# Optimization experiments

Hardware: AMD Instinct MI355X
Metric: run time of the kernel (lower is better)

Reference implementation:

```python
import jax, jax.numpy as jnp
import numpy as np

NC, NW, E, EW = 100000, 500, 600000, 25000
H, L, DFF, CF, WF = 128, 3, 512, 32, 16


def setup_inputs() -> dict:
    key = jax.random.key(0)
    ks = iter(jax.random.split(key, 48))
    def nrm(shape, s=0.05):
        return jax.random.normal(next(ks), shape, jnp.float32) * s
    inp = {}
    inp["cell_x"] = jax.random.normal(next(ks), (NC, CF), jnp.float32)
    inp["well_x"] = jax.random.normal(next(ks), (NW, WF), jnp.float32)
    inp["c2c_edge_index"] = jax.random.randint(next(ks), (2, E), 0, NC)
    inp["c2c_edge_attr"] = jax.random.normal(next(ks), (E, 1), jnp.float32)
    inp["c2w_src"] = jax.random.randint(next(ks), (EW,), 0, NC)
    inp["c2w_dst"] = jax.random.randint(next(ks), (EW,), 0, NW)
    inp["W_cell"] = nrm((CF, H)); inp["b_cell"] = jnp.zeros((H,), jnp.float32)
    inp["W_well"] = nrm((WF, H)); inp["b_well"] = jnp.zeros((H,), jnp.float32)
    inp["W_ee"] = nrm((1, H));   inp["b_ee"] = jnp.zeros((H,), jnp.float32)
    inp["gW"]  = nrm((L, H, H))
    inp["gas"] = nrm((L, H)); inp["gad"] = nrm((L, H)); inp["gae"] = nrm((L, H))
    inp["gWe"] = nrm((L, H, H)); inp["gb"] = jnp.zeros((L, H), jnp.float32)
    inp["n1g"] = jnp.ones((L, H), jnp.float32); inp["n1b"] = jnp.zeros((L, H), jnp.float32)
    inp["fW1"] = nrm((L, H, DFF)); inp["fb1"] = jnp.zeros((L, DFF), jnp.float32)
    inp["fW2"] = nrm((L, DFF, H)); inp["fb2"] = jnp.zeros((L, H), jnp.float32)
    inp["n2g"] = jnp.ones((L, H), jnp.float32); inp["n2b"] = jnp.zeros((L, H), jnp.float32)
    inp["wW"] = nrm((H, H)); inp["was"] = nrm((H,)); inp["wad"] = nrm((H,))
    inp["wb"] = jnp.zeros((H,), jnp.float32)
    inp["mW1"] = nrm((H, H)); inp["mb1"] = jnp.zeros((H,), jnp.float32)
    inp["mW2"] = nrm((H, 75)); inp["mb2"] = jnp.zeros((75,), jnp.float32)
    return inp


def _layer_norm(x, g, b):
    mu = x.mean(-1, keepdims=True)
    v = ((x - mu) ** 2).mean(-1, keepdims=True)
    return (x - mu) * jax.lax.rsqrt(v + 1e-5) * g + b


def _seg_softmax(a, seg, n):
    # numerically stable softmax over edges grouped by destination node
    m = jax.ops.segment_max(a, seg, num_segments=n)
    e = jnp.exp(a - m[seg])
    s = jax.ops.segment_sum(e, seg, num_segments=n)
    s = jnp.where(s == 0, 1.0, s)
    return e / s[seg]


def reference(cell_x, well_x, c2c_edge_index, c2c_edge_attr, c2w_src, c2w_dst,
              W_cell, b_cell, W_well, b_well, W_ee, b_ee,
              gW, gas, gad, gae, gWe, gb,
              n1g, n1b, fW1, fb1, fW2, fb2, n2g, n2b,
              wW, was, wad, wb, mW1, mb1, mW2, mb2):
    src, dst = c2c_edge_index[0], c2c_edge_index[1]
    h = cell_x @ W_cell + b_cell           # [NC, H]
    hw = well_x @ W_well + b_well          # [NW, H]
    ea = c2c_edge_attr @ W_ee + b_ee       # [E, H] embedded edge features
    for i in range(L):
        # GATConv with edge features (heads=1, concat=False, no self loops)
        xn = _layer_norm(h, n1g[i], n1b[i])
        hs = xn @ gW[i]                    # [NC, H]
        alpha = (hs @ gas[i])[src] + (hs @ gad[i])[dst] + (ea @ gWe[i]) @ gae[i]
        alpha = jax.nn.leaky_relu(alpha, 0.2)
        alpha = _seg_softmax(alpha, dst, NC)
        msg = jax.ops.segment_sum(hs[src] * alpha[:, None], dst, num_segments=NC) + gb[i]
        h = h + msg                        # residual (dropout = identity in eval)
        xn = _layer_norm(h, n2g[i], n2b[i])
        h = h + (jax.nn.relu(xn @ fW1[i] + fb1[i]) @ fW2[i] + fb2[i])
    # cell -> well bipartite GATConv (shared lin for src/dst, no edge feats)
    hc = h @ wW                            # [NC, H]
    hwp = hw @ wW                          # [NW, H]
    a = (hc @ was)[c2w_src] + (hwp @ wad)[c2w_dst]
    a = jax.nn.leaky_relu(a, 0.2)
    a = _seg_softmax(a, c2w_dst, NW)
    h_well = jax.ops.segment_sum(hc[c2w_src] * a[:, None], c2w_dst, num_segments=NW) + wb
    out = jax.nn.relu(h_well @ mW1 + mb1) @ mW2 + mb2
    return out.reshape(-1, 3, 25)
```

## Files before the change

### kernel.cpp

```cpp
#include <hip/hip_runtime.h>
#include <hip/hip_bf16.h>

#define NC 100000
#define NW 500
#define NE_CC 600000
#define NE_CW 25000
#define H 128
#define NL 3
#define DFF 512
#define DC 64

typedef __bf16 bf16x8 __attribute__((ext_vector_type(8)));
typedef float f32x4 __attribute__((ext_vector_type(4)));
#define MFMA16(a,b,c) __builtin_amdgcn_mfma_f32_16x16x32_bf16(a,b,c,0,0,0)

__device__ __forceinline__ float wsum(float v){
  #pragma unroll
  for (int o = 32; o; o >>= 1) v += __shfl_xor(v, o, 64);
  return v;
}
__device__ __forceinline__ float gsum16(float v){
  #pragma unroll
  for (int o = 1; o < 16; o <<= 1) v += __shfl_xor(v, o, 64);
  return v;
}
__device__ __forceinline__ float gmax16(float v){
  #pragma unroll
  for (int o = 1; o < 16; o <<= 1) v = fmaxf(v, __shfl_xor(v, o, 64));
  return v;
}

__device__ __forceinline__ void gload16(const void* g, void* l){
  __builtin_amdgcn_global_load_lds(
      (const __attribute__((address_space(1))) void*)g,
      (__attribute__((address_space(3))) void*)l, 16, 0, 0);
}


__global__ void prep_imgGW_k(const float* __restrict__ in, char* __restrict__ img, int nmat){
  int tot = nmat * 16384;
  for (int i = blockIdx.x * 256 + threadIdx.x; i < tot; i += gridDim.x * 256){
    int j = i & 7, lane = (i >> 3) & 63, f = (i >> 9) & 31, l = i >> 14;
    int lr = lane & 15, lk = lane >> 4;
    int ks = f >> 3, nt = f & 7;
    int k = ks * 32 + lk * 8 + j, n = nt * 16 + lr;
    float v = in[(size_t)l * 16384 + (size_t)k * 128 + n];
    *(__hip_bfloat16*)(img + (size_t)l * 32768 + f * 1024 + lane * 16 + j * 2) =
        __float2bfloat16(v);
  }
}
__global__ void prep_imgW1_k(const float* __restrict__ in, char* __restrict__ img){
  int tot = 3 * 65536;
  for (int i = blockIdx.x * 256 + threadIdx.x; i < tot; i += gridDim.x * 256){
    int j = i & 7, lane = (i >> 3) & 63, f = (i >> 9) & 15, ch = (i >> 13) & 7, l = i >> 16;
    int lr = lane & 15, lk = lane >> 4;
    int ks = f >> 2, nt = f & 3;
    int k = ks * 32 + lk * 8 + j, n = ch * 64 + nt * 16 + lr;
    float v = in[(size_t)l * 65536 + (size_t)k * 512 + n];
    *(__hip_bfloat16*)(img + (size_t)(l * 8 + ch) * 16384 + f * 1024 + lane * 16 + j * 2) =
        __float2bfloat16(v);
  }
}
__global__ void prep_imgW2_k(const float* __restrict__ in, char* __restrict__ img){
  int tot = 3 * 65536;
  for (int i = blockIdx.x * 256 + threadIdx.x; i < tot; i += gridDim.x * 256){
    int j = i & 7, lane = (i >> 3) & 63, f = (i >> 9) & 15, ch = (i >> 13) & 7, l = i >> 16;
    int lr = lane & 15, lk = lane >> 4;
    int ks = f >> 3, nt = f & 7;
    int k = ch * 64 + ks * 32 + lk * 8 + j, n = nt * 16 + lr;
    float v = in[(size_t)l * 65536 + (size_t)k * 128 + n];
    *(__hip_bfloat16*)(img + (size_t)(l * 8 + ch) * 16384 + f * 1024 + lane * 16 + j * 2) =
        __float2bfloat16(v);
  }
}

__global__ __launch_bounds__(256) void embed_ln_k(const float* __restrict__ x,
    const float* __restrict__ W, const float* __restrict__ b,
    const float* __restrict__ g, const float* __restrict__ lb,
    float* __restrict__ h, __hip_bfloat16* __restrict__ xn, int M)
{
  int lane = threadIdx.x & 63, wid = threadIdx.x >> 6;
  float w0[32], w1[32];
  #pragma unroll
  for (int k = 0; k < 32; k++){
    w0[k] = W[k * 128 + lane];
    w1[k] = W[k * 128 + 64 + lane];
  }
  float b0 = b[lane], b1 = b[lane + 64];
  float g0 = g[lane], g1 = g[lane + 64];
  float e0 = lb[lane], e1 = lb[lane + 64];
  for (int n = blockIdx.x * 4 + wid; n < M; n += gridDim.x * 4){
    const float4* xr = (const float4*)(x + (size_t)n * 32);
    float xs[32];
    #pragma unroll
    for (int q = 0; q < 8; q++){
      float4 t = xr[q];
      xs[4*q] = t.x; xs[4*q+1] = t.y; xs[4*q+2] = t.z; xs[4*q+3] = t.w;
    }
    float a0 = b0, a1 = b1;
    #pragma unroll
    for (int k = 0; k < 32; k++){ a0 += xs[k] * w0[k]; a1 += xs[k] * w1[k]; }
    h[(size_t)n * H + lane]      = a0;
    h[(size_t)n * H + lane + 64] = a1;
    float mu = wsum(a0 + a1) * (1.f / 128.f);
    float d0 = a0 - mu, d1 = a1 - mu;
    float var = wsum(d0 * d0 + d1 * d1) * (1.f / 128.f);
    float rs = rsqrtf(var + 1e-5f);
    xn[(size_t)n * H + lane]      = __float2bfloat16(d0 * rs * g0 + e0);
    xn[(size_t)n * H + lane + 64] = __float2bfloat16(d1 * rs * g1 + e1);
  }
}

template<int K>
__global__ __launch_bounds__(256) void embed_k(const float* __restrict__ x,
    const float* __restrict__ W, const float* __restrict__ b,
    float* __restrict__ h, int M)
{
  __shared__ float sW[K * 128];
  for (int t = threadIdx.x; t < K * 128; t += 256) sW[t] = W[t];
  __syncthreads();
  int j = threadIdx.x & 127, half = threadIdx.x >> 7;
  float bj = b[j];
  for (int n = blockIdx.x * 2 + half; n < M; n += gridDim.x * 2){
    const float* xr = x + (size_t)n * K;
    float acc = bj;
    #pragma unroll
    for (int k = 0; k < K; k++) acc += xr[k] * sW[k * 128 + j];
    h[(size_t)n * H + j] = acc;
  }
}

__global__ void coeff_k(const float* __restrict__ gWe, const float* __restrict__ gae,
    const float* __restrict__ Wee, const float* __restrict__ bee, float* __restrict__ coeff)
{
  __shared__ float red[4];
  int t = threadIdx.x;
  for (int i = 0; i < NL; i++){
    const float* Wr = gWe + ((size_t)i * H + t) * H;
    const float* ga = gae + (size_t)i * H;
    float w = 0.f;
    for (int k = 0; k < H; k++) w += Wr[k] * ga[k];
    float pc = Wee[t] * w, pd = bee[t] * w;
    pc = wsum(pc); pd = wsum(pd);
    if ((t & 63) == 0){ red[(t >> 6) * 2 + 0] = pc; red[(t >> 6) * 2 + 1] = pd; }
    __syncthreads();
    if (t == 0){ coeff[i] = red[0] + red[2]; coeff[NL + i] = red[1] + red[3]; }
    __syncthreads();
  }
}

__global__ __launch_bounds__(256) void dot2_k(const float* __restrict__ X,
    const float* __restrict__ va, float* __restrict__ oa, int M)
{
  int lane = threadIdx.x & 63, wid = threadIdx.x >> 6;
  int n = blockIdx.x * 4 + wid;
  if (n >= M) return;
  const float* row = X + (size_t)n * H;
  float a = wsum(row[lane] * va[lane] + row[lane + 64] * va[lane + 64]);
  if (lane == 0) oa[n] = a;
}

__global__ __launch_bounds__(512, 4) void gemm_mfma_k(
    const __hip_bfloat16* __restrict__ A, const char* __restrict__ Wimg,
    float* __restrict__ C, __hip_bfloat16* __restrict__ Cbf,
    const float* __restrict__ va, const float* __restrict__ vb,
    float* __restrict__ oa, float* __restrict__ ob, int M)
{
  __shared__ uint4 sW4[2048];
  char* sW = (char*)sW4;
  const int tid = threadIdx.x;
  const int lane = tid & 63, w = tid >> 6;
  const int n0 = blockIdx.x * 128;
  const int rw = w * 16;
  const int lr = lane & 15, lk = lane >> 4;

  {
    int go = w * 1024 + lane * 16;
    #pragma unroll
    for (int q = 0; q < 4; q++)
      gload16(Wimg + q * 8192 + go, sW + q * 8192 + w * 1024);
  }

  const int arow = n0 + rw + lr;
  bf16x8 aX[4];
  if (arow < M){
    #pragma unroll
    for (int ks = 0; ks < 4; ks++)
      aX[ks] = *(const bf16x8*)(A + (size_t)arow * 128 + ks * 32 + lk * 8);
  } else {
    #pragma unroll
    for (int ks = 0; ks < 4; ks++) aX[ks] = (bf16x8){0,0,0,0,0,0,0,0};
  }
  __syncthreads();

  f32x4 acc[8];
  #pragma unroll
  for (int i = 0; i < 8; i++) acc[i] = (f32x4){0.f, 0.f, 0.f, 0.f};
  #pragma unroll
  for (int ks = 0; ks < 4; ks++){
    #pragma unroll
    for (int nt = 0; nt < 8; nt++){
      bf16x8 b = *(const bf16x8*)(sW + ((ks << 3) + nt) * 1024 + (lane << 4));
      acc[nt] = MFMA16(aX[ks], b, acc[nt]);
    }
  }
  #pragma unroll
  for (int nt = 0; nt < 8; nt++){
    int col = nt * 16 + lr;
    #pragma unroll
    for (int r = 0; r < 4; r++){
      int row = n0 + rw + lk * 4 + r;
      if (row < M){
        if (C)   C[(size_t)row * 128 + col] = acc[nt][r];
        if (Cbf) Cbf[(size_t)row * 128 + col] = __float2bfloat16(acc[nt][r]);
      }
    }
  }
  if (va){
    float vac[8], vbc[8];
    #pragma unroll
    for (int nt = 0; nt < 8; nt++){
      vac[nt] = va[nt * 16 + lr];
      vbc[nt] = vb ? vb[nt * 16 + lr] : 0.f;
    }
    #pragma unroll
    for (int r = 0; r < 4; r++){
      float da = 0.f, db = 0.f;
      #pragma unroll
      for (int nt = 0; nt < 8; nt++){
        da += acc[nt][r] * vac[nt];
        db += acc[nt][r] * vbc[nt];
      }
      #pragma unroll
      for (int o = 1; o < 16; o <<= 1){
        da += __shfl_xor(da, o, 64);
        db += __shfl_xor(db, o, 64);
      }
      int row = n0 + rw + lk * 4 + r;
      if (lr == 0 && row < M){
        oa[row] = da;
        if (ob) ob[row] = db;
      }
    }
  }
}

__global__ __launch_bounds__(512, 4) void ffn_mfma_k(
    const __hip_bfloat16* __restrict__ xn, float* __restrict__ h,
    const char* __restrict__ W1img, const float* __restrict__ b1,
    const char* __restrict__ W2img, const float* __restrict__ b2,
    const float* __restrict__ lng, const float* __restrict__ lnb,
    const char* __restrict__ Wg,
    const float* __restrict__ va, const float* __restrict__ vb,
    float* __restrict__ oa, float* __restrict__ ob,
    __hip_bfloat16* __restrict__ Cbf, int mode, int M)
{
  __shared__ uint4 sW1_4[2][1024];
  __shared__ uint4 sW2_4[2][1024];
  __shared__ uint4 sT4[1024];
  char* sT = (char*)sT4;
  const int tid = threadIdx.x;
  const int lane = tid & 63, w = tid >> 6;
  const int n0 = blockIdx.x * 128;
  const int rw = w * 16;
  const int lr = lane & 15, lk = lane >> 4;
  const int go = w * 1024 + lane * 16;
  const int lo = w * 1024;
  char* sTw = sT + w * 2048;

  const int arow = n0 + rw + lr;
  bf16x8 aX[4];
  if (arow < M){
    #pragma unroll
    for (int ks = 0; ks < 4; ks++)
      aX[ks] = *(const bf16x8*)(xn + (size_t)arow * 128 + ks * 32 + lk * 8);
  } else {
    #pragma unroll
    for (int ks = 0; ks < 4; ks++) aX[ks] = (bf16x8){0,0,0,0,0,0,0,0};
  }

  gload16(W1img + go,        (char*)sW1_4[0] + lo);
  gload16(W1img + 8192 + go, (char*)sW1_4[0] + 8192 + lo);
  gload16(W2img + go,        (char*)sW2_4[0] + lo);
  gload16(W2img + 8192 + go, (char*)sW2_4[0] + 8192 + lo);
  asm volatile("s_waitcnt vmcnt(0)" ::: "memory");
  __builtin_amdgcn_s_barrier();

  f32x4 acc2[8];
  #pragma unroll
  for (int i = 0; i < 8; i++) acc2[i] = (f32x4){0.f, 0.f, 0.f, 0.f};

  const int rdA = ((lane ^ ((lane >> 3) & 7)) << 4);

  for (int ch = 0; ch < DFF / DC; ch++){
    const int cur = ch & 1;
    if (ch < DFF / DC - 1){
      const char* g1 = W1img + (size_t)(ch + 1) * 16384;
      const char* g2 = W2img + (size_t)(ch + 1) * 16384;
      char* d1 = (char*)sW1_4[cur ^ 1];
      char* d2 = (char*)sW2_4[cur ^ 1];
      gload16(g1 + go,        d1 + lo);
      gload16(g1 + 8192 + go, d1 + 8192 + lo);
      gload16(g2 + go,        d2 + lo);
      gload16(g2 + 8192 + go, d2 + 8192 + lo);
    } else {
      gload16(Wg + go,         (char*)sW1_4[0] + lo);
      gload16(Wg + 8192 + go,  (char*)sW1_4[0] + 8192 + lo);
      gload16(Wg + 16384 + go, (char*)sW2_4[0] + lo);
      gload16(Wg + 24576 + go, (char*)sW2_4[0] + 8192 + lo);
    }

    const char* W1c = (const char*)sW1_4[cur];
    const char* W2c = (const char*)sW2_4[cur];

    f32x4 acc1[4];
    #pragma unroll
    for (int i = 0; i < 4; i++) acc1[i] = (f32x4){0.f, 0.f, 0.f, 0.f};
    #pragma unroll
    for (int ks = 0; ks < 4; ks++){
      #pragma unroll
      for (int nt = 0; nt < 4; nt++){
        bf16x8 b = *(const bf16x8*)(W1c + ((ks << 2) + nt) * 1024 + (lane << 4));
        acc1[nt] = MFMA16(aX[ks], b, acc1[nt]);
      }
    }
    #pragma unroll
    for (int nt = 0; nt < 4; nt++){
      int col = nt * 16 + lr;
      float bb = b1[ch * DC + col];
      int ksp = col >> 5;
      int qhi = ((col >> 3) & 3) << 4;
      int jb  = (col & 7) << 1;
      #pragma unroll
      for (int r = 0; r < 4; r++){
        int slot = qhi + lk * 4 + r;
        int slotp = slot ^ ((slot >> 3) & 7);
        float v = fmaxf(acc1[nt][r] + bb, 0.f);
        *(__hip_bfloat16*)(sTw + (ksp << 10) + (slotp << 4) + jb) = __float2bfloat16(v);
      }
    }
    asm volatile("s_waitcnt lgkmcnt(0)" ::: "memory");

    #pragma unroll
    for (int ks = 0; ks < 2; ks++){
      bf16x8 a = *(const bf16x8*)(sTw + (ks << 10) + rdA);
      #pragma unroll
      for (int nt = 0; nt < 8; nt++){
        bf16x8 b = *(const bf16x8*)(W2c + ((ks << 3) + nt) * 1024 + (lane << 4));
        acc2[nt] = MFMA16(a, b, acc2[nt]);
      }
    }
    if (ch < DFF / DC - 1){
      asm volatile("s_waitcnt vmcnt(0)" ::: "memory");
      __builtin_amdgcn_s_barrier();
    }
  }

  asm volatile("s_waitcnt vmcnt(0)" ::: "memory");
  __builtin_amdgcn_s_barrier();

  char* aimg = (w < 4) ? ((char*)sW1_4[1] + w * 4096)
                       : ((char*)sW2_4[1] + (w - 4) * 4096);

  float b2c[8];
  #pragma unroll
  for (int nt = 0; nt < 8; nt++) b2c[nt] = b2[nt * 16 + lr];
  float lngc[8], lnbc[8];
  if (mode == 0){
    #pragma unroll
    for (int nt = 0; nt < 8; nt++){
      lngc[nt] = lng[nt * 16 + lr];
      lnbc[nt] = lnb[nt * 16 + lr];
    }
  }

  #pragma unroll
  for (int r = 0; r < 4; r++){
    int row = n0 + rw + lk * 4 + r;
    bool ok = row < M;
    float val[8]; float sum = 0.f;
    #pragma unroll
    for (int nt = 0; nt < 8; nt++){
      int col = nt * 16 + lr;
      float hv = ok ? h[(size_t)row * 128 + col] : 0.f;
      val[nt] = hv + acc2[nt][r] + b2c[nt];
      sum += val[nt];
    }
    float mu = 0.f, rs = 1.f;
    if (mode == 0){
      #pragma unroll
      for (int o = 1; o < 16; o <<= 1) sum += __shfl_xor(sum, o, 64);
      mu = sum * (1.f / 128.f);
      float vs = 0.f;
      #pragma unroll
      for (int nt = 0; nt < 8; nt++){ float d = val[nt] - mu; vs += d * d; }
      #pragma unroll
      for (int o = 1; o < 16; o <<= 1) vs += __shfl_xor(vs, o, 64);
      rs = rsqrtf(vs * (1.f / 128.f) + 1e-5f);
    }
    #pragma unroll
    for (int nt = 0; nt < 8; nt++){
      int col = nt * 16 + lr;
      if (mode == 0 && ok) h[(size_t)row * 128 + col] = val[nt];
      float xo = (mode == 0) ? ((val[nt] - mu) * rs * lngc[nt] + lnbc[nt]) : val[nt];
      int lanep = ((((nt & 1) << 1) + (lr >> 3)) << 4) + (lk << 2) + r;
      *(__hip_bfloat16*)(aimg + ((nt >> 1) << 10) + (lanep << 4) + ((lr & 7) << 1)) =
          __float2bfloat16(xo);
    }
  }
  asm volatile("s_waitcnt lgkmcnt(0)" ::: "memory");

  bf16x8 aG[4];
  #pragma unroll
  for (int ks = 0; ks < 4; ks++)
    aG[ks] = *(const bf16x8*)(aimg + (ks << 10) + (lane << 4));
  f32x4 accG[8];
  #pragma unroll
  for (int i = 0; i < 8; i++) accG[i] = (f32x4){0.f, 0.f, 0.f, 0.f};
  #pragma unroll
  for (int ks = 0; ks < 4; ks++){
    #pragma unroll
    for (int nt = 0; nt < 8; nt++){
      const char* bptr = (ks < 2)
          ? ((const char*)sW1_4[0] + (((ks << 3) + nt) << 10) + (lane << 4))
          : ((const char*)sW2_4[0] + ((((ks - 2) << 3) + nt) << 10) + (lane << 4));
      accG[nt] = MFMA16(aG[ks], *(const bf16x8*)bptr, accG[nt]);
    }
  }
  #pragma unroll
  for (int nt = 0; nt < 8; nt++){
    int col = nt * 16 + lr;
    #pragma unroll
    for (int r = 0; r < 4; r++){
      int row = n0 + rw + lk * 4 + r;
      if (row < M) Cbf[(size_t)row * 128 + col] = __float2bfloat16(accG[nt][r]);
    }
  }
  {
    float vac[8], vbc[8];
    #pragma unroll
    for (int nt = 0; nt < 8; nt++){
      vac[nt] = va[nt * 16 + lr];
      vbc[nt] = vb ? vb[nt * 16 + lr] : 0.f;
    }
    #pragma unroll
    for (int r = 0; r < 4; r++){
      float da = 0.f, db = 0.f;
      #pragma unroll
      for (int nt = 0; nt < 8; nt++){
        da += accG[nt][r] * vac[nt];
        db += accG[nt][r] * vbc[nt];
      }
      #pragma unroll
      for (int o = 1; o < 16; o <<= 1){
        da += __shfl_xor(da, o, 64);
        db += __shfl_xor(db, o, 64);
      }
      int row = n0 + rw + lk * 4 + r;
      if (lr == 0 && row < M){
        oa[row] = da;
        if (ob) ob[row] = db;
      }
    }
  }
}

__global__ __launch_bounds__(256) void gemm128_k(const float* __restrict__ A,
    const float* __restrict__ Bm, float* __restrict__ C, int M)
{
  __shared__ float sB[32 * 128];
  __shared__ float sA[64 * 33];
  const int tid = threadIdx.x;
  const int n0 = blockIdx.x * 64;
  const int j4 = (tid & 31) * 4;
  const int rB = (tid >> 5) * 8;
  float acc[8][4];
  #pragma unroll
  for (int r = 0; r < 8; r++){ acc[r][0]=acc[r][1]=acc[r][2]=acc[r][3]=0.f; }
  for (int kc = 0; kc < 128; kc += 32){
    for (int t = tid; t < 4096; t += 256){
      int kk = t >> 7, j = t & 127;
      sB[kk * 128 + j] = Bm[(size_t)(kc + kk) * H + j];
    }
    for (int t = tid; t < 2048; t += 256){
      int n = t >> 5, kk = t & 31; int row = n0 + n;
      sA[n * 33 + kk] = (row < M) ? A[(size_t)row * H + kc + kk] : 0.f;
    }
    __syncthreads();
    #pragma unroll 8
    for (int kk = 0; kk < 32; kk++){
      float4 bv = *(const float4*)&sB[kk * 128 + j4];
      #pragma unroll
      for (int r = 0; r < 8; r++){
        float av = sA[(rB + r) * 33 + kk];
        acc[r][0] += av * bv.x; acc[r][1] += av * bv.y;
        acc[r][2] += av * bv.z; acc[r][3] += av * bv.w;
      }
    }
    __syncthreads();
  }
  #pragma unroll
  for (int r = 0; r < 8; r++){
    int row = n0 + rB + r;
    if (row < M){
      float4 o; o.x = acc[r][0]; o.y = acc[r][1]; o.z = acc[r][2]; o.w = acc[r][3];
      *(float4*)&C[(size_t)row * H + j4] = o;
    }
  }
}

__global__ void count_k(const int* __restrict__ dst, int* __restrict__ cnt, int NE){
  int e = blockIdx.x * 256 + threadIdx.x;
  if (e < NE) atomicAdd(&cnt[dst[e]], 1);
}
__global__ void scan1_k(const int* __restrict__ in, int* __restrict__ out,
                        int* __restrict__ bsum, int N){
  __shared__ int sd[256];
  int tid = threadIdx.x;
  int base = blockIdx.x * 1024 + tid * 4;
  int v0 = (base + 0 < N) ? in[base + 0] : 0;
  int v1 = (base + 1 < N) ? in[base + 1] : 0;
  int v2 = (base + 2 < N) ? in[base + 2] : 0;
  int v3 = (base + 3 < N) ? in[base + 3] : 0;
  sd[tid] = v0 + v1 + v2 + v3;
  __syncthreads();
  for (int off = 1; off < 256; off <<= 1){
    int t = (tid >= off) ? sd[tid - off] : 0;
    __syncthreads();
    sd[tid] += t;
    __syncthreads();
  }
  int run = (tid > 0) ? sd[tid - 1] : 0;
  run += v0; if (base + 0 < N) out[base + 0] = run;
  run += v1; if (base + 1 < N) out[base + 1] = run;
  run += v2; if (base + 2 < N) out[base + 2] = run;
  run += v3; if (base + 3 < N) out[base + 3] = run;
  if (tid == 255) bsum[blockIdx.x] = sd[255];
}
__global__ void scan2_k(int* __restrict__ bs, int NB){
  __shared__ int sd[256];
  int tid = threadIdx.x;
  int base = tid * 4;
  int v0 = (base + 0 < NB) ? bs[base + 0] : 0;
  int v1 = (base + 1 < NB) ? bs[base + 1] : 0;
  int v2 = (base + 2 < NB) ? bs[base + 2] : 0;
  int v3 = (base + 3 < NB) ? bs[base + 3] : 0;
  sd[tid] = v0 + v1 + v2 + v3;
  __syncthreads();
  for (int off = 1; off < 256; off <<= 1){
    int t = (tid >= off) ? sd[tid - off] : 0;
    __syncthreads();
    sd[tid] += t;
    __syncthreads();
  }
  int run = (tid > 0) ? sd[tid - 1] : 0;
  run += v0; if (base + 0 < NB) bs[base + 0] = run;
  run += v1; if (base + 1 < NB) bs[base + 1] = run;
  run += v2; if (base + 2 < NB) bs[base + 2] = run;
  run += v3; if (base + 3 < NB) bs[base + 3] = run;
}
__global__ void scan3_k(int* __restrict__ out, const int* __restrict__ bsum, int N){
  int b = blockIdx.x;
  if (b == 0) return;
  int add = bsum[b - 1];
  int i = b * 1024 + threadIdx.x * 4;
  #pragma unroll
  for (int j = 0; j < 4; j++) if (i + j < N) out[i + j] += add;
}
__global__ void initfill_k(const int* __restrict__ incl, int* __restrict__ fill, int N){
  int i = blockIdx.x * 256 + threadIdx.x;
  if (i < N) fill[i] = (i == 0) ? 0 : incl[i - 1];
}
__global__ void fill_k(const int* __restrict__ dst, int* __restrict__ fill,
                       int* __restrict__ csr, int NE){
  int e = blockIdx.x * 256 + threadIdx.x;
  if (e < NE){
    int p = atomicAdd(&fill[dst[e]], 1);
    csr[p] = e;
  }
}

__global__ __launch_bounds__(256) void gat_k(
    const int* __restrict__ incl, const int* __restrict__ csr,
    const int* __restrict__ src, const float* __restrict__ attr,
    const float* __restrict__ coeff, int ci,
    const float* __restrict__ as_, const float* __restrict__ ad_,
    const __hip_bfloat16* __restrict__ X, float* __restrict__ hout,
    const float* __restrict__ gb, const float* __restrict__ g,
    const float* __restrict__ b, __hip_bfloat16* __restrict__ xn,
    int M, int residual)
{
  int lane = threadIdx.x & 63, wid = threadIdx.x >> 6;
  int grp = lane >> 4, gl = lane & 15;
  int n = blockIdx.x * 16 + wid * 4 + grp;
  if (n >= M) return;
  int beg = (n == 0) ? 0 : incl[n - 1];
  int end = incl[n];
  float c0 = 0.f, c1 = 0.f;
  if (attr){ c0 = coeff[ci]; c1 = coeff[NL + ci]; }
  float adn = ad_[n];
  const int gbase = grp << 4;
  float m = -1e30f, s = 0.f;
  float acc[8];
  #pragma unroll
  for (int i = 0; i < 8; i++) acc[i] = 0.f;

#define GACC(U, P) \
    acc[0] += (P) * __uint_as_float((U).x << 16); \
    acc[1] += (P) * __uint_as_float((U).x & 0xffff0000u); \
    acc[2] += (P) * __uint_as_float((U).y << 16); \
    acc[3] += (P) * __uint_as_float((U).y & 0xffff0000u); \
    acc[4] += (P) * __uint_as_float((U).z << 16); \
    acc[5] += (P) * __uint_as_float((U).z & 0xffff0000u); \
    acc[6] += (P) * __uint_as_float((U).w << 16); \
    acc[7] += (P) * __uint_as_float((U).w & 0xffff0000u);

  for (int base = beg; base < end; base += 16){
    int idx = base + gl;
    bool valid = idx < end;
    int e = valid ? csr[idx] : 0;
    int sv = valid ? src[e] : 0;
    float a = -1e30f;
    if (valid){
      a = as_[sv] + adn;
      if (attr) a += attr[e] * c0 + c1;
      a = (a > 0.f) ? a : 0.2f * a;
    }
    float cm = gmax16(a);
    float nm = fmaxf(m, cm);
    float sc = expf(m - nm);
    #pragma unroll
    for (int i = 0; i < 8; i++) acc[i] *= sc;
    s *= sc;
    float p = valid ? expf(a - nm) : 0.f;
    s += gsum16(p);
    m = nm;
    int cnt = min(16, end - base);
    int t = 0;
    for (; t + 4 <= cnt; t += 4){
      float p0 = __shfl(p, gbase + t + 0, 64);
      float p1 = __shfl(p, gbase + t + 1, 64);
      float p2 = __shfl(p, gbase + t + 2, 64);
      float p3 = __shfl(p, gbase + t + 3, 64);
      int s0 = __shfl(sv, gbase + t + 0, 64);
      int s1 = __shfl(sv, gbase + t + 1, 64);
      int s2 = __shfl(sv, gbase + t + 2, 64);
      int s3 = __shfl(sv, gbase + t + 3, 64);
      uint4 u0 = *(const uint4*)(X + (size_t)s0 * H + gl * 8);
      uint4 u1 = *(const uint4*)(X + (size_t)s1 * H + gl * 8);
      uint4 u2 = *(const uint4*)(X + (size_t)s2 * H + gl * 8);
      uint4 u3 = *(const uint4*)(X + (size_t)s3 * H + gl * 8);
      GACC(u0, p0) GACC(u1, p1) GACC(u2, p2) GACC(u3, p3)
    }
    if (t + 2 <= cnt){
      float p0 = __shfl(p, gbase + t + 0, 64);
      float p1 = __shfl(p, gbase + t + 1, 64);
      int s0 = __shfl(sv, gbase + t + 0, 64);
      int s1 = __shfl(sv, gbase + t + 1, 64);
      uint4 u0 = *(const uint4*)(X + (size_t)s0 * H + gl * 8);
      uint4 u1 = *(const uint4*)(X + (size_t)s1 * H + gl * 8);
      GACC(u0, p0) GACC(u1, p1)
      t += 2;
    }
    if (t < cnt){
      float p0 = __shfl(p, gbase + t, 64);
      int s0 = __shfl(sv, gbase + t, 64);
      uint4 u0 = *(const uint4*)(X + (size_t)s0 * H + gl * 8);
      GACC(u0, p0)
    }
  }
#undef GACC
  float inv = (s == 0.f) ? 0.f : 1.f / s;
  int j0 = gl * 8;
  if (residual){
    float4 h0 = *(float4*)&hout[(size_t)n * H + j0];
    float4 h1 = *(float4*)&hout[(size_t)n * H + j0 + 4];
    float4 g0 = *(const float4*)&gb[j0];
    float4 g1 = *(const float4*)&gb[j0 + 4];
    float hv[8];
    hv[0] = h0.x + acc[0] * inv + g0.x; hv[1] = h0.y + acc[1] * inv + g0.y;
    hv[2] = h0.z + acc[2] * inv + g0.z; hv[3] = h0.w + acc[3] * inv + g0.w;
    hv[4] = h1.x + acc[4] * inv + g1.x; hv[5] = h1.y + acc[5] * inv + g1.y;
    hv[6] = h1.z + acc[6] * inv + g1.z; hv[7] = h1.w + acc[7] * inv + g1.w;
    float localsum = 0.f;
    #pragma unroll
    for (int i = 0; i < 8; i++) localsum += hv[i];
    float mu = gsum16(localsum) * (1.f / H);
    float vs = 0.f;
    #pragma unroll
    for (int i = 0; i < 8; i++){ float d = hv[i] - mu; vs += d * d; }
    float var = gsum16(vs) * (1.f / H);
    float rs = rsqrtf(var + 1e-5f);
    float4 o0, o1;
    o0.x = hv[0]; o0.y = hv[1]; o0.z = hv[2]; o0.w = hv[3];
    o1.x = hv[4]; o1.y = hv[5]; o1.z = hv[6]; o1.w = hv[7];
    *(float4*)&hout[(size_t)n * H + j0] = o0;
    *(float4*)&hout[(size_t)n * H + j0 + 4] = o1;
    float4 gg0 = *(const float4*)&g[j0];
    float4 gg1 = *(const float4*)&g[j0 + 4];
    float4 bb0 = *(const float4*)&b[j0];
    float4 bb1 = *(const float4*)&b[j0 + 4];
    float xo[8];
    xo[0] = (hv[0]-mu)*rs*gg0.x + bb0.x; xo[1] = (hv[1]-mu)*rs*gg0.y + bb0.y;
    xo[2] = (hv[2]-mu)*rs*gg0.z + bb0.z; xo[3] = (hv[3]-mu)*rs*gg0.w + bb0.w;
    xo[4] = (hv[4]-mu)*rs*gg1.x + bb1.x; xo[5] = (hv[5]-mu)*rs*gg1.y + bb1.y;
    xo[6] = (hv[6]-mu)*rs*gg1.z + bb1.z; xo[7] = (hv[7]-mu)*rs*gg1.w + bb1.w;
    uint4 ow;
    unsigned* owp = (unsigned*)&ow;
    #pragma unroll
    for (int i = 0; i < 4; i++){
      __hip_bfloat16 lo = __float2bfloat16(xo[2*i]);
      __hip_bfloat16 hi = __float2bfloat16(xo[2*i+1]);
      owp[i] = ((unsigned)(*(unsigned short*)&hi) << 16) | (*(unsigned short*)&lo);
    }
    *(uint4*)((char*)xn + ((size_t)n * H + j0) * 2) = ow;
  } else {
    float4 o0, o1;
    o0.x = acc[0]*inv; o0.y = acc[1]*inv; o0.z = acc[2]*inv; o0.w = acc[3]*inv;
    o1.x = acc[4]*inv; o1.y = acc[5]*inv; o1.z = acc[6]*inv; o1.w = acc[7]*inv;
    *(float4*)&hout[(size_t)n * H + j0] = o0;
    *(float4*)&hout[(size_t)n * H + j0 + 4] = o1;
  }
}

__global__ __launch_bounds__(128) void mlp_k(const float* __restrict__ hwell,
    const float* __restrict__ wb, const float* __restrict__ mW1,
    const float* __restrict__ mb1, const float* __restrict__ mW2,
    const float* __restrict__ mb2, float* __restrict__ out)
{
  __shared__ float sH[128], sT[128];
  int n = blockIdx.x, j = threadIdx.x;
  sH[j] = hwell[(size_t)n * H + j] + wb[j];
  __syncthreads();
  float a = mb1[j];
  for (int k = 0; k < 128; k++) a += sH[k] * mW1[k * 128 + j];
  sT[j] = fmaxf(a, 0.f);
  __syncthreads();
  if (j < 75){
    float o = mb2[j];
    for (int k = 0; k < 128; k++) o += sT[k] * mW2[k * 75 + j];
    out[(size_t)n * 75 + j] = o;
  }
}

extern "C" void kernel_launch(void* const* d_in, const int* in_sizes, int n_in,
                              void* d_out, int out_size, void* d_ws, size_t ws_size,
                              hipStream_t stream)
{
  (void)in_sizes; (void)n_in; (void)out_size; (void)ws_size;
  const float* cell_x = (const float*)d_in[0];
  const float* well_x = (const float*)d_in[1];
  const int*   eidx   = (const int*)d_in[2];
  const float* eattr  = (const float*)d_in[3];
  const int*   wsrc   = (const int*)d_in[4];
  const int*   wdst   = (const int*)d_in[5];
  const float* W_cell = (const float*)d_in[6];
  const float* b_cell = (const float*)d_in[7];
  const float* W_well = (const float*)d_in[8];
  const float* b_well = (const float*)d_in[9];
  const float* W_ee   = (const float*)d_in[10];
  const float* b_ee   = (const float*)d_in[11];
  const float* gW     = (const float*)d_in[12];
  const float* gas    = (const float*)d_in[13];
  const float* gad    = (const float*)d_in[14];
  const float* gae    = (const float*)d_in[15];
  const float* gWe    = (const float*)d_in[16];
  const float* gb     = (const float*)d_in[17];
  const float* n1g    = (const float*)d_in[18];
  const float* n1b    = (const float*)d_in[19];
  const float* fW1    = (const float*)d_in[20];
  const float* fb1    = (const float*)d_in[21];
  const float* fW2    = (const float*)d_in[22];
  const float* fb2    = (const float*)d_in[23];
  const float* n2g    = (const float*)d_in[24];
  const float* n2b    = (const float*)d_in[25];
  const float* wW     = (const float*)d_in[26];
  const float* was    = (const float*)d_in[27];
  const float* wad    = (const float*)d_in[28];
  const float* wb     = (const float*)d_in[29];
  const float* mW1    = (const float*)d_in[30];
  const float* mb1    = (const float*)d_in[31];
  const float* mW2    = (const float*)d_in[32];
  const float* mb2    = (const float*)d_in[33];

  const int* src = eidx;
  const int* dst = eidx + NE_CC;

  char* wsb = (char*)d_ws;
  size_t off = 0;
  auto alloc = [&](size_t bytes) -> void* {
    void* p = wsb + off; off += (bytes + 255) & ~(size_t)255; return p;
  };
  float* h      = (float*)alloc((size_t)NC * H * 4);
  __hip_bfloat16* xnbf = (__hip_bfloat16*)alloc((size_t)NC * H * 2);
  __hip_bfloat16* hsbf = (__hip_bfloat16*)alloc((size_t)NC * H * 2);
  float* as_    = (float*)alloc((size_t)NC * 4);
  float* ad_    = (float*)alloc((size_t)NC * 4);
  float* hw     = (float*)alloc((size_t)NW * H * 4);
  float* hwp    = (float*)alloc((size_t)NW * H * 4);
  float* hwell  = (float*)alloc((size_t)NW * H * 4);
  float* coeff  = (float*)alloc(64);
  char* gWimg = (char*)alloc((size_t)NL * 32768);
  char* wWimg = (char*)alloc(32768);
  char* W1img = (char*)alloc((size_t)NL * 131072);
  char* W2img = (char*)alloc((size_t)NL * 131072);
  int* cntC  = (int*)alloc((size_t)NC * 4);
  int* inclC = (int*)alloc((size_t)NC * 4);
  int* fillC = (int*)alloc((size_t)NC * 4);
  int* csrC  = (int*)alloc((size_t)NE_CC * 4);
  int* inclW = (int*)alloc((size_t)NW * 4);
  int* fillW = (int*)alloc((size_t)NW * 4);
  int* csrW  = (int*)alloc((size_t)NE_CW * 4);
  int* bsum  = (int*)alloc(1024 * 4);

  const int eBlocks  = (NE_CC + 255) / 256;
  const int ewBlocks = (NE_CW + 255) / 256;
  const int NBC = (NC + 1023) / 1024;
  const int NBW = (NW + 1023) / 1024;

  hipMemsetAsync(cntC, 0, (size_t)NC * 4, stream);
  count_k<<<eBlocks, 256, 0, stream>>>(dst, cntC, NE_CC);
  scan1_k<<<NBC, 256, 0, stream>>>(cntC, inclC, bsum, NC);
  scan2_k<<<1, 256, 0, stream>>>(bsum, NBC);
  scan3_k<<<NBC, 256, 0, stream>>>(inclC, bsum, NC);
  initfill_k<<<(NC + 255) / 256, 256, 0, stream>>>(inclC, fillC, NC);
  fill_k<<<eBlocks, 256, 0, stream>>>(dst, fillC, csrC, NE_CC);
  hipMemsetAsync(fillW, 0, (size_t)NW * 4, stream);
  count_k<<<ewBlocks, 256, 0, stream>>>(wdst, fillW, NE_CW);
  scan1_k<<<NBW, 256, 0, stream>>>(fillW, inclW, bsum, NW);
  scan2_k<<<1, 256, 0, stream>>>(bsum, NBW);
  scan3_k<<<NBW, 256, 0, stream>>>(inclW, bsum, NW);
  initfill_k<<<(NW + 255) / 256, 256, 0, stream>>>(inclW, fillW, NW);
  fill_k<<<ewBlocks, 256, 0, stream>>>(wdst, fillW, csrW, NE_CW);

  prep_imgGW_k<<<96, 256, 0, stream>>>(gW, gWimg, NL);
  prep_imgGW_k<<<32, 256, 0, stream>>>(wW, wWimg, 1);
  prep_imgW1_k<<<768, 256, 0, stream>>>(fW1, W1img);
  prep_imgW2_k<<<768, 256, 0, stream>>>(fW2, W2img);

  embed_ln_k<<<1024, 256, 0, stream>>>(cell_x, W_cell, b_cell, n1g, n1b, h, xnbf, NC);
  embed_k<16><<<250, 256, 0, stream>>>(well_x, W_well, b_well, hw, NW);
  coeff_k<<<1, 128, 0, stream>>>(gWe, gae, W_ee, b_ee, coeff);

  const int mfmaBlocks = (NC + 127) / 128;
  const int gatBlocks = (NC + 15) / 16;

  gemm_mfma_k<<<mfmaBlocks, 512, 0, stream>>>(xnbf, gWimg,
      nullptr, hsbf, gas, gad, as_, ad_, NC);

  for (int i = 0; i < NL; i++){
    gat_k<<<gatBlocks, 256, 0, stream>>>(inclC, csrC, src, eattr, coeff, i,
        as_, ad_, hsbf, h, gb + i * H, n2g + i * H, n2b + i * H, xnbf, NC, 1);
    if (i < NL - 1){
      ffn_mfma_k<<<mfmaBlocks, 512, 0, stream>>>(xnbf, h,
          W1img + (size_t)i * 131072, fb1 + (size_t)i * DFF,
          W2img + (size_t)i * 131072, fb2 + (size_t)i * H,
          n1g + (i + 1) * H, n1b + (i + 1) * H,
          gWimg + (size_t)(i + 1) * 32768,
          gas + (i + 1) * H, gad + (i + 1) * H, as_, ad_, hsbf, 0, NC);
    } else {
      ffn_mfma_k<<<mfmaBlocks, 512, 0, stream>>>(xnbf, h,
          W1img + (size_t)i * 131072, fb1 + (size_t)i * DFF,
          W2img + (size_t)i * 131072, fb2 + (size_t)i * H,
          n1g, n1b,
          wWimg, was, nullptr, as_, nullptr, hsbf, 1, NC);
    }
  }

  gemm128_k<<<(NW + 63) / 64, 256, 0, stream>>>(hw, wW, hwp, NW);
  dot2_k<<<(NW + 3) / 4, 256, 0, stream>>>(hwp, wad, ad_, NW);
  gat_k<<<(NW + 15) / 16, 256, 0, stream>>>(inclW, csrW, wsrc, nullptr, coeff, 0,
      as_, ad_, hsbf, hwell, nullptr, nullptr, nullptr, nullptr, NW, 0);
  mlp_k<<<NW, 128, 0, stream>>>(hwell, wb, mW1, mb1, mW2, mb2, (float*)d_out);
}
```

Before: 600.4 us.

## Fuse GAT aggregation and LayerNorm into the FFN MFMA kernel with ping-pong buffers

The per-layer GAT edge aggregation, residual add and second LayerNorm now run inside the FFN MFMA kernel. The normalized bf16 tile goes straight to shared memory as the MFMA A operand instead of a round trip through global memory and a separate launch. Because the fused kernel reads neighbor features while writing the next layer's features, hs and the attention score arrays are double-buffered. The aggregation phase now uses the 512-thread MFMA block, with each wave handling 16 nodes, which may lower occupancy or overlap during the irregular gather.

```diff
diff --git a/kernel.cpp b/kernel.cpp
--- a/kernel.cpp
+++ b/kernel.cpp
@@ -35,7 +35,6 @@
       (const __attribute__((address_space(1))) void*)g,
       (__attribute__((address_space(3))) void*)l, 16, 0, 0);
 }
-
 
 __global__ void prep_imgGW_k(const float* __restrict__ in, char* __restrict__ img, int nmat){
   int tot = nmat * 16384;
@@ -162,7 +161,7 @@
 
 __global__ __launch_bounds__(512, 4) void gemm_mfma_k(
     const __hip_bfloat16* __restrict__ A, const char* __restrict__ Wimg,
-    float* __restrict__ C, __hip_bfloat16* __restrict__ Cbf,
+    __hip_bfloat16* __restrict__ Cbf,
     const float* __restrict__ va, const float* __restrict__ vb,
     float* __restrict__ oa, float* __restrict__ ob, int M)
 {
@@ -210,13 +209,10 @@
     #pragma unroll
     for (int r = 0; r < 4; r++){
       int row = n0 + rw + lk * 4 + r;
-      if (row < M){
-        if (C)   C[(size_t)row * 128 + col] = acc[nt][r];
-        if (Cbf) Cbf[(size_t)row * 128 + col] = __float2bfloat16(acc[nt][r]);
-      }
-    }
-  }
-  if (va){
+      if (row < M) Cbf[(size_t)row * 128 + col] = __float2bfloat16(acc[nt][r]);
+    }
+  }
+  {
     float vac[8], vbc[8];
     #pragma unroll
     for (int nt = 0; nt < 8; nt++){
@@ -245,8 +241,15 @@
   }
 }
 
-__global__ __launch_bounds__(512, 4) void ffn_mfma_k(
-    const __hip_bfloat16* __restrict__ xn, float* __restrict__ h,
+__global__ __launch_bounds__(512, 4) void mega_k(
+    const int* __restrict__ incl, const int* __restrict__ csr,
+    const int* __restrict__ src, const float* __restrict__ attr,
+    const float* __restrict__ coeff, int ci,
+    const float* __restrict__ as_in, const float* __restrict__ ad_in,
+    const __hip_bfloat16* __restrict__ X,
+    const float* __restrict__ gbv,
+    const float* __restrict__ n2gv, const float* __restrict__ n2bv,
+    float* __restrict__ h,
     const char* __restrict__ W1img, const float* __restrict__ b1,
     const char* __restrict__ W2img, const float* __restrict__ b2,
     const float* __restrict__ lng, const float* __restrict__ lnb,
@@ -264,26 +267,149 @@
   const int n0 = blockIdx.x * 128;
   const int rw = w * 16;
   const int lr = lane & 15, lk = lane >> 4;
+  const int gl = lane & 15, grp = lane >> 4;
   const int go = w * 1024 + lane * 16;
   const int lo = w * 1024;
   char* sTw = sT + w * 2048;
-
-  const int arow = n0 + rw + lr;
-  bf16x8 aX[4];
-  if (arow < M){
-    #pragma unroll
-    for (int ks = 0; ks < 4; ks++)
-      aX[ks] = *(const bf16x8*)(xn + (size_t)arow * 128 + ks * 32 + lk * 8);
-  } else {
-    #pragma unroll
-    for (int ks = 0; ks < 4; ks++) aX[ks] = (bf16x8){0,0,0,0,0,0,0,0};
-  }
+  char* aimgW = (w < 4) ? ((char*)sW1_4[1] + w * 4096)
+                        : ((char*)sW2_4[1] + (w - 4) * 4096);
 
   gload16(W1img + go,        (char*)sW1_4[0] + lo);
   gload16(W1img + 8192 + go, (char*)sW1_4[0] + 8192 + lo);
   gload16(W2img + go,        (char*)sW2_4[0] + lo);
   gload16(W2img + 8192 + go, (char*)sW2_4[0] + 8192 + lo);
-  asm volatile("s_waitcnt vmcnt(0)" ::: "memory");
+
+  const float c0 = coeff[ci], c1 = coeff[NL + ci];
+  const int gbase = grp << 4;
+#define GACC(U, P) \
+    acc[0] += (P) * __uint_as_float((U).x << 16); \
+    acc[1] += (P) * __uint_as_float((U).x & 0xffff0000u); \
+    acc[2] += (P) * __uint_as_float((U).y << 16); \
+    acc[3] += (P) * __uint_as_float((U).y & 0xffff0000u); \
+    acc[4] += (P) * __uint_as_float((U).z << 16); \
+    acc[5] += (P) * __uint_as_float((U).z & 0xffff0000u); \
+    acc[6] += (P) * __uint_as_float((U).w << 16); \
+    acc[7] += (P) * __uint_as_float((U).w & 0xffff0000u);
+
+  for (int q = 0; q < 4; q++){
+    int n = n0 + w * 16 + grp * 4 + q;
+    char* adst = aimgW + ((gl >> 2) << 10) + ((((gl & 3) << 4) + grp * 4 + q) << 4);
+    if (n >= M){
+      *(uint4*)adst = make_uint4(0u, 0u, 0u, 0u);
+      continue;
+    }
+    int beg = (n == 0) ? 0 : incl[n - 1];
+    int end = incl[n];
+    float adn = ad_in[n];
+    float m = -1e30f, s = 0.f;
+    float acc[8];
+    #pragma unroll
+    for (int i = 0; i < 8; i++) acc[i] = 0.f;
+    for (int base = beg; base < end; base += 16){
+      int idx = base + gl;
+      bool valid = idx < end;
+      int e = valid ? csr[idx] : 0;
+      int sv = valid ? src[e] : 0;
+      float a = -1e30f;
+      if (valid){
+        a = as_in[sv] + adn + attr[e] * c0 + c1;
+        a = (a > 0.f) ? a : 0.2f * a;
+      }
+      float cm = gmax16(a);
+      float nm = fmaxf(m, cm);
+      float sc = expf(m - nm);
+      #pragma unroll
+      for (int i = 0; i < 8; i++) acc[i] *= sc;
+      s *= sc;
+      float p = valid ? expf(a - nm) : 0.f;
+      s += gsum16(p);
+      m = nm;
+      int cnt = min(16, end - base);
+      int t = 0;
+      for (; t + 4 <= cnt; t += 4){
+        float p0 = __shfl(p, gbase + t + 0, 64);
+        float p1 = __shfl(p, gbase + t + 1, 64);
+        float p2 = __shfl(p, gbase + t + 2, 64);
+        float p3 = __shfl(p, gbase + t + 3, 64);
+        int s0 = __shfl(sv, gbase + t + 0, 64);
+        int s1 = __shfl(sv, gbase + t + 1, 64);
+        int s2 = __shfl(sv, gbase + t + 2, 64);
+        int s3 = __shfl(sv, gbase + t + 3, 64);
+        uint4 u0 = *(const uint4*)(X + (size_t)s0 * H + gl * 8);
+        uint4 u1 = *(const uint4*)(X + (size_t)s1 * H + gl * 8);
+        uint4 u2 = *(const uint4*)(X + (size_t)s2 * H + gl * 8);
+        uint4 u3 = *(const uint4*)(X + (size_t)s3 * H + gl * 8);
+        GACC(u0, p0) GACC(u1, p1) GACC(u2, p2) GACC(u3, p3)
+      }
+      if (t + 2 <= cnt){
+        float p0 = __shfl(p, gbase + t + 0, 64);
+        float p1 = __shfl(p, gbase + t + 1, 64);
+        int s0 = __shfl(sv, gbase + t + 0, 64);
+        int s1 = __shfl(sv, gbase + t + 1, 64);
+        uint4 u0 = *(const uint4*)(X + (size_t)s0 * H + gl * 8);
+        uint4 u1 = *(const uint4*)(X + (size_t)s1 * H + gl * 8);
+        GACC(u0, p0) GACC(u1, p1)
+        t += 2;
+      }
+      if (t < cnt){
+        float p0 = __shfl(p, gbase + t, 64);
+        int s0 = __shfl(sv, gbase + t, 64);
+        uint4 u0 = *(const uint4*)(X + (size_t)s0 * H + gl * 8);
+        GACC(u0, p0)
+      }
+    }
+    float inv = (s == 0.f) ? 0.f : 1.f / s;
+    int j0 = gl * 8;
+    float4 h0 = *(float4*)&h[(size_t)n * H + j0];
+    float4 h1 = *(float4*)&h[(size_t)n * H + j0 + 4];
+    float4 g0 = *(const float4*)&gbv[j0];
+    float4 g1 = *(const float4*)&gbv[j0 + 4];
+    float hv[8];
+    hv[0] = h0.x + acc[0] * inv + g0.x; hv[1] = h0.y + acc[1] * inv + g0.y;
+    hv[2] = h0.z + acc[2] * inv + g0.z; hv[3] = h0.w + acc[3] * inv + g0.w;
+    hv[4] = h1.x + acc[4] * inv + g1.x; hv[5] = h1.y + acc[5] * inv + g1.y;
+    hv[6] = h1.z + acc[6] * inv + g1.z; hv[7] = h1.w + acc[7] * inv + g1.w;
+    float localsum = 0.f;
+    #pragma unroll
+    for (int i = 0; i < 8; i++) localsum += hv[i];
+    float mu = gsum16(localsum) * (1.f / H);
+    float vs = 0.f;
+    #pragma unroll
+    for (int i = 0; i < 8; i++){ float d = hv[i] - mu; vs += d * d; }
+    float var = gsum16(vs) * (1.f / H);
+    float rs = rsqrtf(var + 1e-5f);
+    float4 o0, o1;
+    o0.x = hv[0]; o0.y = hv[1]; o0.z = hv[2]; o0.w = hv[3];
+    o1.x = hv[4]; o1.y = hv[5]; o1.z = hv[6]; o1.w = hv[7];
+    *(float4*)&h[(size_t)n * H + j0] = o0;
+    *(float4*)&h[(size_t)n * H + j0 + 4] = o1;
+    float4 gg0 = *(const float4*)&n2gv[j0];
+    float4 gg1 = *(const float4*)&n2gv[j0 + 4];
+    float4 bb0 = *(const float4*)&n2bv[j0];
+    float4 bb1 = *(const float4*)&n2bv[j0 + 4];
+    float xo[8];
+    xo[0] = (hv[0]-mu)*rs*gg0.x + bb0.x; xo[1] = (hv[1]-mu)*rs*gg0.y + bb0.y;
+    xo[2] = (hv[2]-mu)*rs*gg0.z + bb0.z; xo[3] = (hv[3]-mu)*rs*gg0.w + bb0.w;
+    xo[4] = (hv[4]-mu)*rs*gg1.x + bb1.x; xo[5] = (hv[5]-mu)*rs*gg1.y + bb1.y;
+    xo[6] = (hv[6]-mu)*rs*gg1.z + bb1.z; xo[7] = (hv[7]-mu)*rs*gg1.w + bb1.w;
+    uint4 ow;
+    unsigned* owp = (unsigned*)&ow;
+    #pragma unroll
+    for (int i = 0; i < 4; i++){
+      __hip_bfloat16 lo2 = __float2bfloat16(xo[2*i]);
+      __hip_bfloat16 hi2 = __float2bfloat16(xo[2*i+1]);
+      owp[i] = ((unsigned)(*(unsigned short*)&hi2) << 16) | (*(unsigned short*)&lo2);
+    }
+    *(uint4*)adst = ow;
+  }
+#undef GACC
+
+  asm volatile("s_waitcnt lgkmcnt(0)" ::: "memory");
+  bf16x8 aX[4];
+  #pragma unroll
+  for (int ks = 0; ks < 4; ks++)
+    aX[ks] = *(const bf16x8*)(aimgW + (ks << 10) + (lane << 4));
+  asm volatile("s_waitcnt lgkmcnt(0) vmcnt(0)" ::: "memory");
   __builtin_amdgcn_s_barrier();
 
   f32x4 acc2[8];
@@ -359,9 +485,6 @@
   asm volatile("s_waitcnt vmcnt(0)" ::: "memory");
   __builtin_amdgcn_s_barrier();
 
-  char* aimg = (w < 4) ? ((char*)sW1_4[1] + w * 4096)
-                       : ((char*)sW2_4[1] + (w - 4) * 4096);
-
   float b2c[8];
   #pragma unroll
   for (int nt = 0; nt < 8; nt++) b2c[nt] = b2[nt * 16 + lr];
@@ -404,7 +527,7 @@
       if (mode == 0 && ok) h[(size_t)row * 128 + col] = val[nt];
       float xo = (mode == 0) ? ((val[nt] - mu) * rs * lngc[nt] + lnbc[nt]) : val[nt];
       int lanep = ((((nt & 1) << 1) + (lr >> 3)) << 4) + (lk << 2) + r;
-      *(__hip_bfloat16*)(aimg + ((nt >> 1) << 10) + (lanep << 4) + ((lr & 7) << 1)) =
+      *(__hip_bfloat16*)(aimgW + ((nt >> 1) << 10) + (lanep << 4) + ((lr & 7) << 1)) =
           __float2bfloat16(xo);
     }
   }
@@ -413,7 +536,7 @@
   bf16x8 aG[4];
   #pragma unroll
   for (int ks = 0; ks < 4; ks++)
-    aG[ks] = *(const bf16x8*)(aimg + (ks << 10) + (lane << 4));
+    aG[ks] = *(const bf16x8*)(aimgW + (ks << 10) + (lane << 4));
   f32x4 accG[8];
   #pragma unroll
   for (int i = 0; i < 8; i++) accG[i] = (f32x4){0.f, 0.f, 0.f, 0.f};
@@ -582,13 +705,9 @@
 
 __global__ __launch_bounds__(256) void gat_k(
     const int* __restrict__ incl, const int* __restrict__ csr,
-    const int* __restrict__ src, const float* __restrict__ attr,
-    const float* __restrict__ coeff, int ci,
+    const int* __restrict__ src,
     const float* __restrict__ as_, const float* __restrict__ ad_,
-    const __hip_bfloat16* __restrict__ X, float* __restrict__ hout,
-    const float* __restrict__ gb, const float* __restrict__ g,
-    const float* __restrict__ b, __hip_bfloat16* __restrict__ xn,
-    int M, int residual)
+    const __hip_bfloat16* __restrict__ X, float* __restrict__ hout, int M)
 {
   int lane = threadIdx.x & 63, wid = threadIdx.x >> 6;
   int grp = lane >> 4, gl = lane & 15;
@@ -596,15 +715,12 @@
   if (n >= M) return;
   int beg = (n == 0) ? 0 : incl[n - 1];
   int end = incl[n];
-  float c0 = 0.f, c1 = 0.f;
-  if (attr){ c0 = coeff[ci]; c1 = coeff[NL + ci]; }
   float adn = ad_[n];
   const int gbase = grp << 4;
   float m = -1e30f, s = 0.f;
   float acc[8];
   #pragma unroll
   for (int i = 0; i < 8; i++) acc[i] = 0.f;
-
 #define GACC(U, P) \
     acc[0] += (P) * __uint_as_float((U).x << 16); \
     acc[1] += (P) * __uint_as_float((U).x & 0xffff0000u); \
@@ -614,7 +730,6 @@
     acc[5] += (P) * __uint_as_float((U).z & 0xffff0000u); \
     acc[6] += (P) * __uint_as_float((U).w << 16); \
     acc[7] += (P) * __uint_as_float((U).w & 0xffff0000u);
-
   for (int base = beg; base < end; base += 16){
     int idx = base + gl;
     bool valid = idx < end;
@@ -623,7 +738,6 @@
     float a = -1e30f;
     if (valid){
       a = as_[sv] + adn;
-      if (attr) a += attr[e] * c0 + c1;
       a = (a > 0.f) ? a : 0.2f * a;
     }
     float cm = gmax16(a);
@@ -636,91 +750,21 @@
     s += gsum16(p);
     m = nm;
     int cnt = min(16, end - base);
-    int t = 0;
-    for (; t + 4 <= cnt; t += 4){
-      float p0 = __shfl(p, gbase + t + 0, 64);
-      float p1 = __shfl(p, gbase + t + 1, 64);
-      float p2 = __shfl(p, gbase + t + 2, 64);
-      float p3 = __shfl(p, gbase + t + 3, 64);
-      int s0 = __shfl(sv, gbase + t + 0, 64);
-      int s1 = __shfl(sv, gbase + t + 1, 64);
-      int s2 = __shfl(sv, gbase + t + 2, 64);
-      int s3 = __shfl(sv, gbase + t + 3, 64);
-      uint4 u0 = *(const uint4*)(X + (size_t)s0 * H + gl * 8);
-      uint4 u1 = *(const uint4*)(X + (size_t)s1 * H + gl * 8);
-      uint4 u2 = *(const uint4*)(X + (size_t)s2 * H + gl * 8);
-      uint4 u3 = *(const uint4*)(X + (size_t)s3 * H + gl * 8);
-      GACC(u0, p0) GACC(u1, p1) GACC(u2, p2) GACC(u3, p3)
-    }
-    if (t + 2 <= cnt){
-      float p0 = __shfl(p, gbase + t + 0, 64);
-      float p1 = __shfl(p, gbase + t + 1, 64);
-      int s0 = __shfl(sv, gbase + t + 0, 64);
-      int s1 = __shfl(sv, gbase + t + 1, 64);
-      uint4 u0 = *(const uint4*)(X + (size_t)s0 * H + gl * 8);
-      uint4 u1 = *(const uint4*)(X + (size_t)s1 * H + gl * 8);
-      GACC(u0, p0) GACC(u1, p1)
-      t += 2;
-    }
-    if (t < cnt){
-      float p0 = __shfl(p, gbase + t, 64);
-      int s0 = __shfl(sv, gbase + t, 64);
-      uint4 u0 = *(const uint4*)(X + (size_t)s0 * H + gl * 8);
-      GACC(u0, p0)
+    for (int t = 0; t < cnt; t++){
+      float pt = __shfl(p, gbase + t, 64);
+      int st = __shfl(sv, gbase + t, 64);
+      uint4 u = *(const uint4*)(X + (size_t)st * H + gl * 8);
+      GACC(u, pt)
     }
   }
 #undef GACC
   float inv = (s == 0.f) ? 0.f : 1.f / s;
   int j0 = gl * 8;
-  if (residual){
-    float4 h0 = *(float4*)&hout[(size_t)n * H + j0];
-    float4 h1 = *(float4*)&hout[(size_t)n * H + j0 + 4];
-    float4 g0 = *(const float4*)&gb[j0];
-    float4 g1 = *(const float4*)&gb[j0 + 4];
-    float hv[8];
-    hv[0] = h0.x + acc[0] * inv + g0.x; hv[1] = h0.y + acc[1] * inv + g0.y;
-    hv[2] = h0.z + acc[2] * inv + g0.z; hv[3] = h0.w + acc[3] * inv + g0.w;
-    hv[4] = h1.x + acc[4] * inv + g1.x; hv[5] = h1.y + acc[5] * inv + g1.y;
-    hv[6] = h1.z + acc[6] * inv + g1.z; hv[7] = h1.w + acc[7] * inv + g1.w;
-    float localsum = 0.f;
-    #pragma unroll
-    for (int i = 0; i < 8; i++) localsum += hv[i];
-    float mu = gsum16(localsum) * (1.f / H);
-    float vs = 0.f;
-    #pragma unroll
-    for (int i = 0; i < 8; i++){ float d = hv[i] - mu; vs += d * d; }
-    float var = gsum16(vs) * (1.f / H);
-    float rs = rsqrtf(var + 1e-5f);
-    float4 o0, o1;
-    o0.x = hv[0]; o0.y = hv[1]; o0.z = hv[2]; o0.w = hv[3];
-    o1.x = hv[4]; o1.y = hv[5]; o1.z = hv[6]; o1.w = hv[7];
-    *(float4*)&hout[(size_t)n * H + j0] = o0;
-    *(float4*)&hout[(size_t)n * H + j0 + 4] = o1;
-    float4 gg0 = *(const float4*)&g[j0];
-    float4 gg1 = *(const float4*)&g[j0 + 4];
-    float4 bb0 = *(const float4*)&b[j0];
-    float4 bb1 = *(const float4*)&b[j0 + 4];
-    float xo[8];
-    xo[0] = (hv[0]-mu)*rs*gg0.x + bb0.x; xo[1] = (hv[1]-mu)*rs*gg0.y + bb0.y;
-    xo[2] = (hv[2]-mu)*rs*gg0.z + bb0.z; xo[3] = (hv[3]-mu)*rs*gg0.w + bb0.w;
-    xo[4] = (hv[4]-mu)*rs*gg1.x + bb1.x; xo[5] = (hv[5]-mu)*rs*gg1.y + bb1.y;
-    xo[6] = (hv[6]-mu)*rs*gg1.z + bb1.z; xo[7] = (hv[7]-mu)*rs*gg1.w + bb1.w;
-    uint4 ow;
-    unsigned* owp = (unsigned*)&ow;
-    #pragma unroll
-    for (int i = 0; i < 4; i++){
-      __hip_bfloat16 lo = __float2bfloat16(xo[2*i]);
-      __hip_bfloat16 hi = __float2bfloat16(xo[2*i+1]);
-      owp[i] = ((unsigned)(*(unsigned short*)&hi) << 16) | (*(unsigned short*)&lo);
-    }
-    *(uint4*)((char*)xn + ((size_t)n * H + j0) * 2) = ow;
-  } else {
-    float4 o0, o1;
-    o0.x = acc[0]*inv; o0.y = acc[1]*inv; o0.z = acc[2]*inv; o0.w = acc[3]*inv;
-    o1.x = acc[4]*inv; o1.y = acc[5]*inv; o1.z = acc[6]*inv; o1.w = acc[7]*inv;
-    *(float4*)&hout[(size_t)n * H + j0] = o0;
-    *(float4*)&hout[(size_t)n * H + j0 + 4] = o1;
-  }
+  float4 o0, o1;
+  o0.x = acc[0]*inv; o0.y = acc[1]*inv; o0.z = acc[2]*inv; o0.w = acc[3]*inv;
+  o1.x = acc[4]*inv; o1.y = acc[5]*inv; o1.z = acc[6]*inv; o1.w = acc[7]*inv;
+  *(float4*)&hout[(size_t)n * H + j0] = o0;
+  *(float4*)&hout[(size_t)n * H + j0 + 4] = o1;
 }
 
 __global__ __launch_bounds__(128) void mlp_k(const float* __restrict__ hwell,
@@ -792,10 +836,13 @@
     void* p = wsb + off; off += (bytes + 255) & ~(size_t)255; return p;
   };
   float* h      = (float*)alloc((size_t)NC * H * 4);
-  __hip_bfloat16* xnbf = (__hip_bfloat16*)alloc((size_t)NC * H * 2);
-  __hip_bfloat16* hsbf = (__hip_bfloat16*)alloc((size_t)NC * H * 2);
-  float* as_    = (float*)alloc((size_t)NC * 4);
-  float* ad_    = (float*)alloc((size_t)NC * 4);
+  __hip_bfloat16* xnbf  = (__hip_bfloat16*)alloc((size_t)NC * H * 2);
+  __hip_bfloat16* hsbf0 = (__hip_bfloat16*)alloc((size_t)NC * H * 2);
+  __hip_bfloat16* hsbf1 = (__hip_bfloat16*)alloc((size_t)NC * H * 2);
+  float* as0    = (float*)alloc((size_t)NC * 4);
+  float* ad0    = (float*)alloc((size_t)NC * 4);
+  float* as1    = (float*)alloc((size_t)NC * 4);
+  float* ad1    = (float*)alloc((size_t)NC * 4);
   float* hw     = (float*)alloc((size_t)NW * H * 4);
   float* hwp    = (float*)alloc((size_t)NW * H * 4);
   float* hwell  = (float*)alloc((size_t)NW * H * 4);
@@ -843,33 +890,38 @@
   coeff_k<<<1, 128, 0, stream>>>(gWe, gae, W_ee, b_ee, coeff);
 
   const int mfmaBlocks = (NC + 127) / 128;
-  const int gatBlocks = (NC + 15) / 16;
 
   gemm_mfma_k<<<mfmaBlocks, 512, 0, stream>>>(xnbf, gWimg,
-      nullptr, hsbf, gas, gad, as_, ad_, NC);
+      hsbf0, gas, gad, as0, ad0, NC);
 
   for (int i = 0; i < NL; i++){
-    gat_k<<<gatBlocks, 256, 0, stream>>>(inclC, csrC, src, eattr, coeff, i,
-        as_, ad_, hsbf, h, gb + i * H, n2g + i * H, n2b + i * H, xnbf, NC, 1);
+    const __hip_bfloat16* Xin = (i & 1) ? hsbf1 : hsbf0;
+    __hip_bfloat16* Xout      = (i & 1) ? hsbf0 : hsbf1;
+    const float* asi = (i & 1) ? as1 : as0;
+    const float* adi = (i & 1) ? ad1 : ad0;
+    float* aso = (i & 1) ? as0 : as1;
+    float* ado = (i & 1) ? ad0 : ad1;
     if (i < NL - 1){
-      ffn_mfma_k<<<mfmaBlocks, 512, 0, stream>>>(xnbf, h,
+      mega_k<<<mfmaBlocks, 512, 0, stream>>>(inclC, csrC, src, eattr, coeff, i,
+          asi, adi, Xin, gb + i * H, n2g + i * H, n2b + i * H, h,
           W1img + (size_t)i * 131072, fb1 + (size_t)i * DFF,
           W2img + (size_t)i * 131072, fb2 + (size_t)i * H,
           n1g + (i + 1) * H, n1b + (i + 1) * H,
           gWimg + (size_t)(i + 1) * 32768,
-          gas + (i + 1) * H, gad + (i + 1) * H, as_, ad_, hsbf, 0, NC);
+          gas + (i + 1) * H, gad + (i + 1) * H, aso, ado, Xout, 0, NC);
     } else {
-      ffn_mfma_k<<<mfmaBlocks, 512, 0, stream>>>(xnbf, h,
+      mega_k<<<mfmaBlocks, 512, 0, stream>>>(inclC, csrC, src, eattr, coeff, i,
+          asi, adi, Xin, gb + i * H, n2g + i * H, n2b + i * H, h,
           W1img + (size_t)i * 131072, fb1 + (size_t)i * DFF,
           W2img + (size_t)i * 131072, fb2 + (size_t)i * H,
           n1g, n1b,
-          wWimg, was, nullptr, as_, nullptr, hsbf, 1, NC);
+          wWimg, was, nullptr, aso, nullptr, Xout, 1, NC);
     }
   }
 
   gemm128_k<<<(NW + 63) / 64, 256, 0, stream>>>(hw, wW, hwp, NW);
-  dot2_k<<<(NW + 3) / 4, 256, 0, stream>>>(hwp, wad, ad_, NW);
-  gat_k<<<(NW + 15) / 16, 256, 0, stream>>>(inclW, csrW, wsrc, nullptr, coeff, 0,
-      as_, ad_, hsbf, hwell, nullptr, nullptr, nullptr, nullptr, NW, 0);
+  dot2_k<<<(NW + 3) / 4, 256, 0, stream>>>(hwp, wad, ad0, NW);
+  gat_k<<<(NW + 15) / 16, 256, 0, stream>>>(inclW, csrW, wsrc,
+      as1, ad0, hsbf1, hwell, NW);
   mlp_k<<<NW, 128, 0, stream>>>(hwell, wb, mW1, mb1, mW2, mb2, (float*)d_out);
 }
```

New measurement: 600.1 us. Within noise of the previous version (-0.0%).
